# Performance work log

Measured on AMD Instinct MI355X. Metric: run time of the kernel, lower is better.

## Reference

```python
import jax, jax.numpy as jnp
import numpy as np

N_NODES = 100000

def setup_inputs() -> dict:
    key = jax.random.key(0)
    k1, k2, k3, k4 = jax.random.split(key, 4)
    E = 1600000
    x = jax.random.normal(k1, (N_NODES, 128), dtype=jnp.float32)
    src = jax.random.randint(k2, (E,), 0, N_NODES, dtype=jnp.int32)
    dst = jax.random.randint(k3, (E,), 0, N_NODES, dtype=jnp.int32)
    W = jax.random.normal(k4, (128, 128), dtype=jnp.float32) * (1.0 / np.sqrt(128.0))
    b = jnp.zeros((128,), dtype=jnp.float32)
    return {"x": x, "src": src, "dst": dst, "W": W, "b": b}

def reference(x, src, dst, W, b):
    # DGL GraphConv, norm='both', allow_zero_in_degree=True
    N = x.shape[0]
    ones = jnp.ones_like(src, dtype=x.dtype)
    out_deg = jax.ops.segment_sum(ones, src, num_segments=N)
    in_deg = jax.ops.segment_sum(ones, dst, num_segments=N)
    out_norm = jnp.power(jnp.clip(out_deg, 1.0), -0.5)  # [N]
    in_norm = jnp.power(jnp.clip(in_deg, 1.0), -0.5)    # [N]
    h = x * out_norm[:, None]                            # [N, d]
    msg = h[src]                                         # [E, d] gather
    agg = jax.ops.segment_sum(msg, dst, num_segments=N)  # [N, d] scatter-sum
    agg = agg * in_norm[:, None]
    return agg @ W + b
```

## Files before the change

### kernel.cpp

```cpp
#include <hip/hip_runtime.h>

#define NFEAT 128
#define BSHIFT 9
#define BNODES 512
#define NBMAX 256
#define BCAP 9216
#define CHUNK 4096

typedef __attribute__((ext_vector_type(8))) short bf16x8;
typedef __attribute__((ext_vector_type(4))) float f32x4;
typedef unsigned short u16;

__device__ inline u16 f2bf(float f) {
    unsigned u = __float_as_uint(f);
    u += 0x7FFF + ((u >> 16) & 1);
    return (u16)(u >> 16);
}
__device__ inline float bf2f(u16 h) {
    return __uint_as_float((unsigned)h << 16);
}

__global__ __launch_bounds__(512)
void partition_kernel(const int* __restrict__ src, const int* __restrict__ dst, int E,
                      int* __restrict__ cursor, int* __restrict__ packed,
                      int* __restrict__ out_deg, int NB) {
    __shared__ int cnt[NBMAX];
    __shared__ int loff[NBMAX];
    __shared__ int gbase[NBMAX];
    __shared__ int sa[NBMAX], sb[NBMAX];
    __shared__ int sortv[CHUNK];
    __shared__ u16 sortb[CHUNK];

    int tid = threadIdx.x;
    if (tid < NBMAX) cnt[tid] = 0;
    __syncthreads();

    int base = blockIdx.x * CHUNK;
    int endj = min(base + CHUNK, E);
    int ccnt = endj - base;

    for (int j = base + tid; j < endj; j += 512) {
        atomicAdd(&out_deg[src[j]], 1);
        atomicAdd(&cnt[dst[j] >> BSHIFT], 1);
    }
    __syncthreads();

    int v = (tid < NBMAX) ? cnt[tid] : 0;
    if (tid < NBMAX) sa[tid] = v;
    __syncthreads();
    int* s = sa; int* t = sb;
    for (int d = 1; d < NBMAX; d <<= 1) {
        if (tid < NBMAX) t[tid] = s[tid] + (tid >= d ? s[tid - d] : 0);
        __syncthreads();
        int* tmp = s; s = t; t = tmp;
    }
    if (tid < NBMAX) {
        int excl = s[tid] - v;
        loff[tid] = excl;
        cnt[tid] = excl;
        gbase[tid] = v ? (tid * BCAP + atomicAdd(&cursor[tid], v)) : 0;
    }
    __syncthreads();

    for (int j = base + tid; j < endj; j += 512) {
        int d_ = dst[j];
        int bkt = d_ >> BSHIFT;
        int pos = atomicAdd(&cnt[bkt], 1);
        sortv[pos] = ((d_ & (BNODES - 1)) << 17) | src[j];
        sortb[pos] = (u16)bkt;
    }
    __syncthreads();

    for (int p = tid; p < ccnt; p += 512) {
        int bkt = sortb[p];
        packed[gbase[bkt] + (p - loff[bkt])] = sortv[p];
    }
}

__global__ __launch_bounds__(512)
void fill_cast_kernel(const int* __restrict__ packed, const int* __restrict__ cursor,
                      int* __restrict__ row_start, float* __restrict__ inorm,
                      int* __restrict__ csr_src,
                      const float* __restrict__ x, const int* __restrict__ out_deg,
                      u16* __restrict__ xh, const float* __restrict__ W,
                      u16* __restrict__ Wt, int N, int E, int NB, int nbc) {
    int bid = blockIdx.x;
    int tid = threadIdx.x;

    if (bid < NB) {
        __shared__ int cnt[BNODES];
        __shared__ int sa[BNODES], sb[BNODES];
        __shared__ int ca[256], cb[256];
        int bkt = bid;
        int node0 = bkt << BSHIFT;
        int nn = min(BNODES, N - node0);
        int beg = bkt * BCAP;
        int ccnt = cursor[bkt];

        if (tid < 256) ca[tid] = (tid < NB) ? cursor[tid] : 0;
        __syncthreads();
        int* p = ca; int* q = cb;
        for (int d = 1; d < 256; d <<= 1) {
            if (tid < 256) q[tid] = p[tid] + (tid >= d ? p[tid - d] : 0);
            __syncthreads();
            int* tmp = p; p = q; q = tmp;
        }
        int csr0 = (bkt > 0) ? p[bkt - 1] : 0;
        if (bkt == 0 && tid == 0) row_start[N] = p[NB - 1];

        cnt[tid] = 0;
        __syncthreads();
        for (int i = tid; i < ccnt; i += 512)
            atomicAdd(&cnt[packed[beg + i] >> 17], 1);
        __syncthreads();

        int v = cnt[tid];
        sa[tid] = v;
        __syncthreads();
        int* s = sa; int* t = sb;
        for (int d = 1; d < 512; d <<= 1) {
            t[tid] = s[tid] + (tid >= d ? s[tid - d] : 0);
            __syncthreads();
            int* tmp = s; s = t; t = tmp;
        }
        int excl = s[tid] - v;

        if (tid < nn) {
            row_start[node0 + tid] = csr0 + excl;
            inorm[node0 + tid] = rsqrtf((float)max(v, 1));
        }
        __syncthreads();

        cnt[tid] = csr0 + excl;
        __syncthreads();
        for (int i = tid; i < ccnt; i += 512) {
            int pk = packed[beg + i];
            int slot = atomicAdd(&cnt[pk >> 17], 1);
            csr_src[slot] = pk & 0x1FFFF;
        }
    } else if (bid < NB + nbc) {
        int node0 = (bid - NB) << 7;
        for (int i = tid; i < 128 * 32; i += 512) {
            int r = i >> 5, f4 = i & 31;
            int n = node0 + r;
            if (n >= N) break;
            float sc = rsqrtf((float)max(out_deg[n], 1));
            float4 vv = *reinterpret_cast<const float4*>(&x[(size_t)n * NFEAT + f4 * 4]);
            ushort4 o;
            o.x = f2bf(vv.x * sc); o.y = f2bf(vv.y * sc);
            o.z = f2bf(vv.z * sc); o.w = f2bf(vv.w * sc);
            *reinterpret_cast<ushort4*>(&xh[(size_t)n * NFEAT + f4 * 4]) = o;
        }
    } else {
        for (int i = tid; i < NFEAT * NFEAT; i += 512) {
            int col = i >> 7, k = i & 127;
            Wt[i] = f2bf(W[k * NFEAT + col]);
        }
    }
}

__global__ __launch_bounds__(256)
void agg_bf16_kernel(const u16* __restrict__ xh, const int* __restrict__ csr_src,
                     const int* __restrict__ row_start, const float* __restrict__ inorm,
                     u16* __restrict__ aggh, int N) {
    int node = blockIdx.x * 8 + (threadIdx.x >> 5);
    if (node >= N) return;
    int lf = threadIdx.x & 31;
    int beg = row_start[node];
    int end = row_start[node + 1];
    const ushort4* xr = reinterpret_cast<const ushort4*>(xh);

    float4 acc = make_float4(0.f, 0.f, 0.f, 0.f);
    for (int i = beg; i < end; i += 8) {
        int s[8];
        float m[8];
        #pragma unroll
        for (int u = 0; u < 8; ++u) {
            int j = i + u;
            bool ok = (j < end);
            s[u] = ok ? csr_src[j] : 0;
            m[u] = ok ? 1.f : 0.f;
        }
        ushort4 v[8];
        #pragma unroll
        for (int u = 0; u < 8; ++u)
            v[u] = xr[(size_t)s[u] * 32 + lf];
        #pragma unroll
        for (int u = 0; u < 8; ++u) {
            acc.x = fmaf(m[u], bf2f(v[u].x), acc.x);
            acc.y = fmaf(m[u], bf2f(v[u].y), acc.y);
            acc.z = fmaf(m[u], bf2f(v[u].z), acc.z);
            acc.w = fmaf(m[u], bf2f(v[u].w), acc.w);
        }
    }
    float in_n = inorm[node];
    ushort4 o;
    o.x = f2bf(acc.x * in_n);
    o.y = f2bf(acc.y * in_n);
    o.z = f2bf(acc.z * in_n);
    o.w = f2bf(acc.w * in_n);
    *reinterpret_cast<ushort4*>(aggh + (size_t)node * 256 + lf * 4) = o;
}

__global__ __launch_bounds__(256)
void mm_mfma_kernel(const u16* __restrict__ aggh, float* outp,
                    const u16* __restrict__ Wt, const float* __restrict__ b, int N) {
    __shared__ u16 Al[NFEAT * NFEAT];
    __shared__ u16 Bl[NFEAT * NFEAT];
    int tid = threadIdx.x;
    int r0 = blockIdx.x * 128;

    for (int c = tid; c < 2048; c += 256) {
        int col = c >> 4, sub = c & 15;
        int slot = sub ^ (col & 7);
        *reinterpret_cast<uint4*>(reinterpret_cast<char*>(Bl) + col * 256 + slot * 16) =
            *reinterpret_cast<const uint4*>(reinterpret_cast<const char*>(Wt) + c * 16);
    }
    for (int c = tid; c < 2048; c += 256) {
        int row = c >> 4, sub = c & 15;
        int grow = min(r0 + row, N - 1);
        int slot = sub ^ (row & 7);
        *reinterpret_cast<uint4*>(reinterpret_cast<char*>(Al) + row * 256 + slot * 16) =
            *reinterpret_cast<const uint4*>(reinterpret_cast<const char*>(aggh) +
                                            (size_t)grow * 512 + sub * 16);
    }
    __syncthreads();

    int lane = tid & 63;
    int wave = tid >> 6;
    int wr = wave >> 1, wc = wave & 1;
    int lrow = lane & 15, hi = lane >> 4;

    f32x4 zero = {0.f, 0.f, 0.f, 0.f};
    f32x4 acc[4][4];
    #pragma unroll
    for (int rt = 0; rt < 4; ++rt)
        #pragma unroll
        for (int ct = 0; ct < 4; ++ct) acc[rt][ct] = zero;

    #pragma unroll
    for (int ks = 0; ks < 4; ++ks) {
        int chunk = ks * 4 + hi;
        bf16x8 af[4], bfr[4];
        #pragma unroll
        for (int rt = 0; rt < 4; ++rt) {
            int row = wr * 64 + rt * 16 + lrow;
            af[rt] = *reinterpret_cast<bf16x8*>(reinterpret_cast<char*>(Al) + row * 256 +
                                                ((chunk ^ (row & 7)) * 16));
        }
        #pragma unroll
        for (int ct = 0; ct < 4; ++ct) {
            int col = wc * 64 + ct * 16 + lrow;
            bfr[ct] = *reinterpret_cast<bf16x8*>(reinterpret_cast<char*>(Bl) + col * 256 +
                                                 ((chunk ^ (col & 7)) * 16));
        }
        #pragma unroll
        for (int rt = 0; rt < 4; ++rt)
            #pragma unroll
            for (int ct = 0; ct < 4; ++ct)
                acc[rt][ct] = __builtin_amdgcn_mfma_f32_16x16x32_bf16(af[rt], bfr[ct],
                                                                     acc[rt][ct], 0, 0, 0);
    }

    #pragma unroll
    for (int ct = 0; ct < 4; ++ct) {
        int col = wc * 64 + ct * 16 + lrow;
        float bias = b[col];
        #pragma unroll
        for (int rt = 0; rt < 4; ++rt) {
            int rbase = r0 + wr * 64 + rt * 16 + hi * 4;
            #pragma unroll
            for (int q = 0; q < 4; ++q) {
                int row = rbase + q;
                if (row < N) outp[(size_t)row * NFEAT + col] = acc[rt][ct][q] + bias;
            }
        }
    }
}

extern "C" void kernel_launch(void* const* d_in, const int* in_sizes, int n_in,
                              void* d_out, int out_size, void* d_ws, size_t ws_size,
                              hipStream_t stream) {
    const float* x   = (const float*)d_in[0];
    const int*   src = (const int*)d_in[1];
    const int*   dst = (const int*)d_in[2];
    const float* W   = (const float*)d_in[3];
    const float* b   = (const float*)d_in[4];

    const int N = in_sizes[0] / NFEAT;
    const int E = in_sizes[1];
    float* out = (float*)d_out;

    const int NB = (N + BNODES - 1) >> BSHIFT;

    int*   out_deg   = (int*)d_ws;
    int*   cursor    = out_deg + N;
    int*   row_start = cursor + NBMAX;
    float* inorm     = (float*)(row_start + (N + 1));
    int*   csr_src   = (int*)(inorm + N);
    u16*   Wt        = (u16*)(csr_src + E);
    u16*   xh        = Wt + NFEAT * NFEAT;

    int* packed = (int*)d_out;

    hipMemsetAsync(d_ws, 0, (size_t)(N + NBMAX) * sizeof(int), stream);

    int nchunk = (E + CHUNK - 1) / CHUNK;
    partition_kernel<<<nchunk, 512, 0, stream>>>(src, dst, E, cursor, packed, out_deg, NB);

    int nbc = (N + 127) >> 7;
    fill_cast_kernel<<<NB + nbc + 1, 512, 0, stream>>>(packed, cursor,
                                                       row_start, inorm, csr_src,
                                                       x, out_deg, xh, W, Wt, N, E, NB, nbc);

    u16* aggh = (u16*)d_out;
    agg_bf16_kernel<<<(N + 7) / 8, 256, 0, stream>>>(xh, csr_src, row_start, inorm, aggh, N);

    mm_mfma_kernel<<<(N + 127) / 128, 256, 0, stream>>>(aggh, out, Wt, b, N);
}
```

Baseline: 216.0 us.

## Shrink dst buckets to 256 nodes and read W directly from global in matmul

Bucket size drops from 512 to 256 nodes, giving 391 buckets, with smaller partition chunks and 256-thread partition blocks. The bucket prefix scans are reworked to have each thread handle two entries so 512 buckets fit a 256-wide scan. The matmul kernel no longer stages W in LDS and loads B fragments straight from global or L2, which halves LDS use per block and may raise occupancy at the cost of repeated global reads. The Wt buffer is also aligned to 32 bytes for the vector loads.

After: 250.2 us. 15.8% more time.

```diff
diff --git a/kernel.cpp b/kernel.cpp
--- a/kernel.cpp
+++ b/kernel.cpp
@@ -1,11 +1,11 @@
 #include <hip/hip_runtime.h>
 
 #define NFEAT 128
-#define BSHIFT 9
-#define BNODES 512
-#define NBMAX 256
-#define BCAP 9216
-#define CHUNK 4096
+#define BSHIFT 8
+#define BNODES 256
+#define NBMAX 512
+#define BCAP 5120
+#define CHUNK 2048
 
 typedef __attribute__((ext_vector_type(8))) short bf16x8;
 typedef __attribute__((ext_vector_type(4))) float f32x4;
@@ -20,49 +20,51 @@
     return __uint_as_float((unsigned)h << 16);
 }
 
-__global__ __launch_bounds__(512)
+__global__ __launch_bounds__(256)
 void partition_kernel(const int* __restrict__ src, const int* __restrict__ dst, int E,
                       int* __restrict__ cursor, int* __restrict__ packed,
                       int* __restrict__ out_deg, int NB) {
     __shared__ int cnt[NBMAX];
     __shared__ int loff[NBMAX];
     __shared__ int gbase[NBMAX];
-    __shared__ int sa[NBMAX], sb[NBMAX];
+    __shared__ int sa[256], sb[256];
     __shared__ int sortv[CHUNK];
     __shared__ u16 sortb[CHUNK];
 
     int tid = threadIdx.x;
-    if (tid < NBMAX) cnt[tid] = 0;
+    cnt[tid] = 0;
+    cnt[tid + 256] = 0;
     __syncthreads();
 
     int base = blockIdx.x * CHUNK;
     int endj = min(base + CHUNK, E);
     int ccnt = endj - base;
 
-    for (int j = base + tid; j < endj; j += 512) {
+    for (int j = base + tid; j < endj; j += 256) {
         atomicAdd(&out_deg[src[j]], 1);
         atomicAdd(&cnt[dst[j] >> BSHIFT], 1);
     }
     __syncthreads();
 
-    int v = (tid < NBMAX) ? cnt[tid] : 0;
-    if (tid < NBMAX) sa[tid] = v;
+    int i0 = 2 * tid, i1 = 2 * tid + 1;
+    int v0 = cnt[i0], v1 = cnt[i1];
+    int pr = v0 + v1;
+    sa[tid] = pr;
     __syncthreads();
     int* s = sa; int* t = sb;
-    for (int d = 1; d < NBMAX; d <<= 1) {
-        if (tid < NBMAX) t[tid] = s[tid] + (tid >= d ? s[tid - d] : 0);
+    for (int d = 1; d < 256; d <<= 1) {
+        t[tid] = s[tid] + (tid >= d ? s[tid - d] : 0);
         __syncthreads();
         int* tmp = s; s = t; t = tmp;
     }
-    if (tid < NBMAX) {
-        int excl = s[tid] - v;
-        loff[tid] = excl;
-        cnt[tid] = excl;
-        gbase[tid] = v ? (tid * BCAP + atomicAdd(&cursor[tid], v)) : 0;
-    }
-    __syncthreads();
-
-    for (int j = base + tid; j < endj; j += 512) {
+    int excl = s[tid] - pr;
+    loff[i0] = excl;      loff[i1] = excl + v0;
+    cnt[i0]  = excl;      cnt[i1]  = excl + v0;
+    gbase[i0] = v0 ? (i0 * BCAP + atomicAdd(&cursor[i0], v0)) : 0;
+    gbase[i1] = v1 ? (i1 * BCAP + atomicAdd(&cursor[i1], v1)) : 0;
+    __syncthreads();
+
+    for (int j = base + tid; j < endj; j += 256) {
         int d_ = dst[j];
         int bkt = d_ >> BSHIFT;
         int pos = atomicAdd(&cnt[bkt], 1);
@@ -71,7 +73,7 @@
     }
     __syncthreads();
 
-    for (int p = tid; p < ccnt; p += 512) {
+    for (int p = tid; p < ccnt; p += 256) {
         int bkt = sortb[p];
         packed[gbase[bkt] + (p - loff[bkt])] = sortv[p];
     }
@@ -89,41 +91,53 @@
 
     if (bid < NB) {
         __shared__ int cnt[BNODES];
-        __shared__ int sa[BNODES], sb[BNODES];
-        __shared__ int ca[256], cb[256];
+        __shared__ int sa[256], sb[256];
+        __shared__ int excl2[NBMAX];
         int bkt = bid;
         int node0 = bkt << BSHIFT;
         int nn = min(BNODES, N - node0);
         int beg = bkt * BCAP;
         int ccnt = cursor[bkt];
 
-        if (tid < 256) ca[tid] = (tid < NB) ? cursor[tid] : 0;
-        __syncthreads();
-        int* p = ca; int* q = cb;
+        int i0 = 2 * tid, i1 = 2 * tid + 1;
+        int v0 = 0, v1 = 0;
+        if (tid < 256) {
+            v0 = (i0 < NB) ? cursor[i0] : 0;
+            v1 = (i1 < NB) ? cursor[i1] : 0;
+            sa[tid] = v0 + v1;
+        }
+        __syncthreads();
+        int* p = sa; int* q = sb;
         for (int d = 1; d < 256; d <<= 1) {
             if (tid < 256) q[tid] = p[tid] + (tid >= d ? p[tid - d] : 0);
             __syncthreads();
             int* tmp = p; p = q; q = tmp;
         }
-        int csr0 = (bkt > 0) ? p[bkt - 1] : 0;
-        if (bkt == 0 && tid == 0) row_start[N] = p[NB - 1];
-
-        cnt[tid] = 0;
+        if (tid < 256) {
+            int e2 = p[tid] - (v0 + v1);
+            excl2[i0] = e2;
+            excl2[i1] = e2 + v0;
+        }
+        __syncthreads();
+        int csr0 = excl2[bkt];
+        if (bkt == 0 && tid == 0) row_start[N] = E;
+
+        if (tid < BNODES) cnt[tid] = 0;
         __syncthreads();
         for (int i = tid; i < ccnt; i += 512)
             atomicAdd(&cnt[packed[beg + i] >> 17], 1);
         __syncthreads();
 
-        int v = cnt[tid];
-        sa[tid] = v;
+        int v = (tid < BNODES) ? cnt[tid] : 0;
+        if (tid < 256) sa[tid] = v;
         __syncthreads();
         int* s = sa; int* t = sb;
-        for (int d = 1; d < 512; d <<= 1) {
-            t[tid] = s[tid] + (tid >= d ? s[tid - d] : 0);
+        for (int d = 1; d < 256; d <<= 1) {
+            if (tid < 256) t[tid] = s[tid] + (tid >= d ? s[tid - d] : 0);
             __syncthreads();
             int* tmp = s; s = t; t = tmp;
         }
-        int excl = s[tid] - v;
+        int excl = (tid < BNODES) ? (s[tid] - v) : 0;
 
         if (tid < nn) {
             row_start[node0 + tid] = csr0 + excl;
@@ -131,7 +145,7 @@
         }
         __syncthreads();
 
-        cnt[tid] = csr0 + excl;
+        if (tid < BNODES) cnt[tid] = csr0 + excl;
         __syncthreads();
         for (int i = tid; i < ccnt; i += 512) {
             int pk = packed[beg + i];
@@ -206,16 +220,9 @@
 void mm_mfma_kernel(const u16* __restrict__ aggh, float* outp,
                     const u16* __restrict__ Wt, const float* __restrict__ b, int N) {
     __shared__ u16 Al[NFEAT * NFEAT];
-    __shared__ u16 Bl[NFEAT * NFEAT];
     int tid = threadIdx.x;
     int r0 = blockIdx.x * 128;
 
-    for (int c = tid; c < 2048; c += 256) {
-        int col = c >> 4, sub = c & 15;
-        int slot = sub ^ (col & 7);
-        *reinterpret_cast<uint4*>(reinterpret_cast<char*>(Bl) + col * 256 + slot * 16) =
-            *reinterpret_cast<const uint4*>(reinterpret_cast<const char*>(Wt) + c * 16);
-    }
     for (int c = tid; c < 2048; c += 256) {
         int row = c >> 4, sub = c & 15;
         int grow = min(r0 + row, N - 1);
@@ -251,8 +258,7 @@
         #pragma unroll
         for (int ct = 0; ct < 4; ++ct) {
             int col = wc * 64 + ct * 16 + lrow;
-            bfr[ct] = *reinterpret_cast<bf16x8*>(reinterpret_cast<char*>(Bl) + col * 256 +
-                                                 ((chunk ^ (col & 7)) * 16));
+            bfr[ct] = *reinterpret_cast<const bf16x8*>(Wt + col * NFEAT + chunk * 8);
         }
         #pragma unroll
         for (int rt = 0; rt < 4; ++rt)
@@ -298,7 +304,8 @@
     int*   row_start = cursor + NBMAX;
     float* inorm     = (float*)(row_start + (N + 1));
     int*   csr_src   = (int*)(inorm + N);
-    u16*   Wt        = (u16*)(csr_src + E);
+    uintptr_t wt_addr = ((uintptr_t)(csr_src + E) + 31) & ~(uintptr_t)31;
+    u16*   Wt        = (u16*)wt_addr;
     u16*   xh        = Wt + NFEAT * NFEAT;
 
     int* packed = (int*)d_out;
@@ -306,7 +313,7 @@
     hipMemsetAsync(d_ws, 0, (size_t)(N + NBMAX) * sizeof(int), stream);
 
     int nchunk = (E + CHUNK - 1) / CHUNK;
-    partition_kernel<<<nchunk, 512, 0, stream>>>(src, dst, E, cursor, packed, out_deg, NB);
+    partition_kernel<<<nchunk, 256, 0, stream>>>(src, dst, E, cursor, packed, out_deg, NB);
 
     int nbc = (N + 127) >> 7;
     fill_cast_kernel<<<NB + nbc + 1, 512, 0, stream>>>(packed, cursor,
```

## Split CSR fill blocks in halves and read W fragments directly from global

Applied to the files above, without the earlier changes.

The CSR fill phase now launches two blocks per bucket. Each block recomputes the bucket's histogram and scan but scatters only the destinations in its half of the 512 nodes, which doubles the parallelism of the serial atomic scatter. Separately, the matmul kernel no longer stages W^T in shared memory and instead loads its B fragments straight from global (cache-resident), halving LDS use per block. Wt is aligned to 32 bytes so those vector loads are aligned. The costs are redundant packed-array reads and histogram work, plus repeated global reads of W from every wave.

Result: slower. 220.4 us (+2.0%).

```diff
diff --git a/kernel.cpp b/kernel.cpp
--- a/kernel.cpp
+++ b/kernel.cpp
@@ -87,13 +87,12 @@
     int bid = blockIdx.x;
     int tid = threadIdx.x;
 
-    if (bid < NB) {
+    if (bid < 2 * NB) {
         __shared__ int cnt[BNODES];
         __shared__ int sa[BNODES], sb[BNODES];
         __shared__ int ca[256], cb[256];
-        int bkt = bid;
-        int node0 = bkt << BSHIFT;
-        int nn = min(BNODES, N - node0);
+        int bkt = bid >> 1;
+        int half = bid & 1;
         int beg = bkt * BCAP;
         int ccnt = cursor[bkt];
 
@@ -106,7 +105,7 @@
             int* tmp = p; p = q; q = tmp;
         }
         int csr0 = (bkt > 0) ? p[bkt - 1] : 0;
-        if (bkt == 0 && tid == 0) row_start[N] = p[NB - 1];
+        if (bkt == 0 && half == 0 && tid == 0) row_start[N] = p[NB - 1];
 
         cnt[tid] = 0;
         __syncthreads();
@@ -125,9 +124,12 @@
         }
         int excl = s[tid] - v;
 
-        if (tid < nn) {
-            row_start[node0 + tid] = csr0 + excl;
-            inorm[node0 + tid] = rsqrtf((float)max(v, 1));
+        if ((tid >> 8) == half) {
+            int n = (bkt << BSHIFT) + tid;
+            if (n < N) {
+                row_start[n] = csr0 + excl;
+                inorm[n] = rsqrtf((float)max(v, 1));
+            }
         }
         __syncthreads();
 
@@ -135,11 +137,14 @@
         __syncthreads();
         for (int i = tid; i < ccnt; i += 512) {
             int pk = packed[beg + i];
-            int slot = atomicAdd(&cnt[pk >> 17], 1);
-            csr_src[slot] = pk & 0x1FFFF;
-        }
-    } else if (bid < NB + nbc) {
-        int node0 = (bid - NB) << 7;
+            int nd = pk >> 17;
+            if ((nd >> 8) == half) {
+                int slot = atomicAdd(&cnt[nd], 1);
+                csr_src[slot] = pk & 0x1FFFF;
+            }
+        }
+    } else if (bid < 2 * NB + nbc) {
+        int node0 = (bid - 2 * NB) << 7;
         for (int i = tid; i < 128 * 32; i += 512) {
             int r = i >> 5, f4 = i & 31;
             int n = node0 + r;
@@ -206,16 +211,9 @@
 void mm_mfma_kernel(const u16* __restrict__ aggh, float* outp,
                     const u16* __restrict__ Wt, const float* __restrict__ b, int N) {
     __shared__ u16 Al[NFEAT * NFEAT];
-    __shared__ u16 Bl[NFEAT * NFEAT];
     int tid = threadIdx.x;
     int r0 = blockIdx.x * 128;
 
-    for (int c = tid; c < 2048; c += 256) {
-        int col = c >> 4, sub = c & 15;
-        int slot = sub ^ (col & 7);
-        *reinterpret_cast<uint4*>(reinterpret_cast<char*>(Bl) + col * 256 + slot * 16) =
-            *reinterpret_cast<const uint4*>(reinterpret_cast<const char*>(Wt) + c * 16);
-    }
     for (int c = tid; c < 2048; c += 256) {
         int row = c >> 4, sub = c & 15;
         int grow = min(r0 + row, N - 1);
@@ -251,8 +249,7 @@
         #pragma unroll
         for (int ct = 0; ct < 4; ++ct) {
             int col = wc * 64 + ct * 16 + lrow;
-            bfr[ct] = *reinterpret_cast<bf16x8*>(reinterpret_cast<char*>(Bl) + col * 256 +
-                                                 ((chunk ^ (col & 7)) * 16));
+            bfr[ct] = *reinterpret_cast<const bf16x8*>(Wt + col * NFEAT + chunk * 8);
         }
         #pragma unroll
         for (int rt = 0; rt < 4; ++rt)
@@ -298,7 +295,8 @@
     int*   row_start = cursor + NBMAX;
     float* inorm     = (float*)(row_start + (N + 1));
     int*   csr_src   = (int*)(inorm + N);
-    u16*   Wt        = (u16*)(csr_src + E);
+    uintptr_t wt_addr = ((uintptr_t)(csr_src + E) + 31) & ~(uintptr_t)31;
+    u16*   Wt        = (u16*)wt_addr;
     u16*   xh        = Wt + NFEAT * NFEAT;
 
     int* packed = (int*)d_out;
@@ -309,9 +307,10 @@
     partition_kernel<<<nchunk, 512, 0, stream>>>(src, dst, E, cursor, packed, out_deg, NB);
 
     int nbc = (N + 127) >> 7;
-    fill_cast_kernel<<<NB + nbc + 1, 512, 0, stream>>>(packed, cursor,
-                                                       row_start, inorm, csr_src,
-                                                       x, out_deg, xh, W, Wt, N, E, NB, nbc);
+    fill_cast_kernel<<<2 * NB + nbc + 1, 512, 0, stream>>>(packed, cursor,
+                                                           row_start, inorm, csr_src,
+                                                           x, out_deg, xh, W, Wt,
+                                                           N, E, NB, nbc);
 
     u16* aggh = (u16*)d_out;
     agg_bf16_kernel<<<(N + 7) / 8, 256, 0, stream>>>(xh, csr_src, row_start, inorm, aggh, N);
```

## Batch edge loads into registers in partition and fill kernels; read W from global

Applied to the files above, without the earlier changes.

The partition kernel now loads each thread's eight src/dst values into registers once and reuses them for degree counting and bucket sorting, instead of reading global memory twice. It also merges the two per-bucket offset arrays into one and shrinks the bucket tag to a byte. The fill kernel caches up to 16 packed entries per thread in registers across its count and scatter passes. The matmul kernel drops the shared-memory copy of W and reads B fragments straight from global memory, cutting LDS use and the staging step at the cost of uncached-layout global reads per wave.

Result: no change. 213.9 us (-1.0%).

```diff
diff --git a/kernel.cpp b/kernel.cpp
--- a/kernel.cpp
+++ b/kernel.cpp
@@ -10,6 +10,7 @@
 typedef __attribute__((ext_vector_type(8))) short bf16x8;
 typedef __attribute__((ext_vector_type(4))) float f32x4;
 typedef unsigned short u16;
+typedef unsigned char u8;
 
 __device__ inline u16 f2bf(float f) {
     unsigned u = __float_as_uint(f);
@@ -25,11 +26,10 @@
                       int* __restrict__ cursor, int* __restrict__ packed,
                       int* __restrict__ out_deg, int NB) {
     __shared__ int cnt[NBMAX];
-    __shared__ int loff[NBMAX];
-    __shared__ int gbase[NBMAX];
+    __shared__ int gml[NBMAX];
     __shared__ int sa[NBMAX], sb[NBMAX];
     __shared__ int sortv[CHUNK];
-    __shared__ u16 sortb[CHUNK];
+    __shared__ u8  sortb[CHUNK];
 
     int tid = threadIdx.x;
     if (tid < NBMAX) cnt[tid] = 0;
@@ -39,9 +39,19 @@
     int endj = min(base + CHUNK, E);
     int ccnt = endj - base;
 
-    for (int j = base + tid; j < endj; j += 512) {
-        atomicAdd(&out_deg[src[j]], 1);
-        atomicAdd(&cnt[dst[j] >> BSHIFT], 1);
+    int rs[8], rd[8];
+    #pragma unroll
+    for (int u = 0; u < 8; ++u) {
+        int j = base + tid + u * 512;
+        if (j < endj) { rd[u] = dst[j]; rs[u] = src[j]; }
+    }
+    #pragma unroll
+    for (int u = 0; u < 8; ++u) {
+        int j = base + tid + u * 512;
+        if (j < endj) {
+            atomicAdd(&out_deg[rs[u]], 1);
+            atomicAdd(&cnt[rd[u] >> BSHIFT], 1);
+        }
     }
     __syncthreads();
 
@@ -56,24 +66,27 @@
     }
     if (tid < NBMAX) {
         int excl = s[tid] - v;
-        loff[tid] = excl;
         cnt[tid] = excl;
-        gbase[tid] = v ? (tid * BCAP + atomicAdd(&cursor[tid], v)) : 0;
-    }
-    __syncthreads();
-
-    for (int j = base + tid; j < endj; j += 512) {
-        int d_ = dst[j];
-        int bkt = d_ >> BSHIFT;
-        int pos = atomicAdd(&cnt[bkt], 1);
-        sortv[pos] = ((d_ & (BNODES - 1)) << 17) | src[j];
-        sortb[pos] = (u16)bkt;
+        int gb = v ? (tid * BCAP + atomicAdd(&cursor[tid], v)) : 0;
+        gml[tid] = gb - excl;
+    }
+    __syncthreads();
+
+    #pragma unroll
+    for (int u = 0; u < 8; ++u) {
+        int j = base + tid + u * 512;
+        if (j < endj) {
+            int bkt = rd[u] >> BSHIFT;
+            int pos = atomicAdd(&cnt[bkt], 1);
+            sortv[pos] = ((rd[u] & (BNODES - 1)) << 17) | rs[u];
+            sortb[pos] = (u8)bkt;
+        }
     }
     __syncthreads();
 
     for (int p = tid; p < ccnt; p += 512) {
         int bkt = sortb[p];
-        packed[gbase[bkt] + (p - loff[bkt])] = sortv[p];
+        packed[gml[bkt] + p] = sortv[p];
     }
 }
 
@@ -106,11 +119,23 @@
             int* tmp = p; p = q; q = tmp;
         }
         int csr0 = (bkt > 0) ? p[bkt - 1] : 0;
-        if (bkt == 0 && tid == 0) row_start[N] = p[NB - 1];
-
+        if (bkt == 0 && tid == 0) row_start[N] = E;
+
+        int rp[16];
+        int nv = min(ccnt, 8192);
         cnt[tid] = 0;
         __syncthreads();
-        for (int i = tid; i < ccnt; i += 512)
+        #pragma unroll
+        for (int u = 0; u < 16; ++u) {
+            int i = tid + u * 512;
+            if (i < nv) rp[u] = packed[beg + i];
+        }
+        #pragma unroll
+        for (int u = 0; u < 16; ++u) {
+            int i = tid + u * 512;
+            if (i < nv) atomicAdd(&cnt[rp[u] >> 17], 1);
+        }
+        for (int i = 8192 + tid; i < ccnt; i += 512)
             atomicAdd(&cnt[packed[beg + i] >> 17], 1);
         __syncthreads();
 
@@ -133,7 +158,15 @@
 
         cnt[tid] = csr0 + excl;
         __syncthreads();
-        for (int i = tid; i < ccnt; i += 512) {
+        #pragma unroll
+        for (int u = 0; u < 16; ++u) {
+            int i = tid + u * 512;
+            if (i < nv) {
+                int slot = atomicAdd(&cnt[rp[u] >> 17], 1);
+                csr_src[slot] = rp[u] & 0x1FFFF;
+            }
+        }
+        for (int i = 8192 + tid; i < ccnt; i += 512) {
             int pk = packed[beg + i];
             int slot = atomicAdd(&cnt[pk >> 17], 1);
             csr_src[slot] = pk & 0x1FFFF;
@@ -206,16 +239,9 @@
 void mm_mfma_kernel(const u16* __restrict__ aggh, float* outp,
                     const u16* __restrict__ Wt, const float* __restrict__ b, int N) {
     __shared__ u16 Al[NFEAT * NFEAT];
-    __shared__ u16 Bl[NFEAT * NFEAT];
     int tid = threadIdx.x;
     int r0 = blockIdx.x * 128;
 
-    for (int c = tid; c < 2048; c += 256) {
-        int col = c >> 4, sub = c & 15;
-        int slot = sub ^ (col & 7);
-        *reinterpret_cast<uint4*>(reinterpret_cast<char*>(Bl) + col * 256 + slot * 16) =
-            *reinterpret_cast<const uint4*>(reinterpret_cast<const char*>(Wt) + c * 16);
-    }
     for (int c = tid; c < 2048; c += 256) {
         int row = c >> 4, sub = c & 15;
         int grow = min(r0 + row, N - 1);
@@ -251,8 +277,7 @@
         #pragma unroll
         for (int ct = 0; ct < 4; ++ct) {
             int col = wc * 64 + ct * 16 + lrow;
-            bfr[ct] = *reinterpret_cast<bf16x8*>(reinterpret_cast<char*>(Bl) + col * 256 +
-                                                 ((chunk ^ (col & 7)) * 16));
+            bfr[ct] = *reinterpret_cast<const bf16x8*>(Wt + col * NFEAT + chunk * 8);
         }
         #pragma unroll
         for (int rt = 0; rt < 4; ++rt)
@@ -298,7 +323,8 @@
     int*   row_start = cursor + NBMAX;
     float* inorm     = (float*)(row_start + (N + 1));
     int*   csr_src   = (int*)(inorm + N);
-    u16*   Wt        = (u16*)(csr_src + E);
+    uintptr_t wt_addr = ((uintptr_t)(csr_src + E) + 31) & ~(uintptr_t)31;
+    u16*   Wt        = (u16*)wt_addr;
     u16*   xh        = Wt + NFEAT * NFEAT;
 
     int* packed = (int*)d_out;
@@ -311,7 +337,8 @@
     int nbc = (N + 127) >> 7;
     fill_cast_kernel<<<NB + nbc + 1, 512, 0, stream>>>(packed, cursor,
                                                        row_start, inorm, csr_src,
-                                                       x, out_deg, xh, W, Wt, N, E, NB, nbc);
+                                                       x, out_deg, xh, W, Wt,
+                                                       N, E, NB, nbc);
 
     u16* aggh = (u16*)d_out;
     agg_bf16_kernel<<<(N + 7) / 8, 256, 0, stream>>>(xh, csr_src, row_start, inorm, aggh, N);
```
